# Performance work log

Hardware: AMD Instinct MI355X
Metric: run time of the kernel (lower is better)

The kernel has to match this reference:

```python
import jax, jax.numpy as jnp
import numpy as np

N, E, H, D, L, R = 50000, 800000, 128, 512, 3, 3
BN_EPS = 1e-5


def setup_inputs() -> dict:
    key = jax.random.key(0)
    ks = jax.random.split(key, 10)
    x = jax.random.normal(ks[0], (N, H), jnp.float32)
    edge_src = jax.random.randint(ks[1], (R, E), 0, N, jnp.int32)
    edge_dst = jax.random.randint(ks[2], (R, E), 0, N, jnp.int32)
    conv_W = jax.random.normal(ks[3], (L, R, H, H), jnp.float32) * 0.05
    conv_b = jnp.zeros((L, R, H), jnp.float32)
    fc_W = jax.random.normal(ks[4], (L - 1, H, H), jnp.float32) * 0.05
    fc_b = jnp.zeros((L - 1, H), jnp.float32)
    fc_W_last = jax.random.normal(ks[5], (H, D), jnp.float32) * 0.05
    fc_b_last = jnp.zeros((D,), jnp.float32)
    bn_gamma = jnp.ones((L - 1, H), jnp.float32)
    bn_beta = jnp.zeros((L - 1, H), jnp.float32)
    bn_mean = jax.random.normal(ks[6], (L - 1, H), jnp.float32) * 0.1
    bn_var = jax.random.uniform(ks[7], (L - 1, H), jnp.float32, 0.5, 1.5)
    return {"x": x, "edge_src": edge_src, "edge_dst": edge_dst,
            "conv_W": conv_W, "conv_b": conv_b, "fc_W": fc_W, "fc_b": fc_b,
            "fc_W_last": fc_W_last, "fc_b_last": fc_b_last,
            "bn_gamma": bn_gamma, "bn_beta": bn_beta,
            "bn_mean": bn_mean, "bn_var": bn_var}


def _deg_norm(idx, n, dtype):
    # symmetric GCN norm: 1/sqrt(clamp(deg,1))  (DGL norm='both')
    deg = jax.ops.segment_sum(jnp.ones(idx.shape, dtype), idx, num_segments=n)
    return jax.lax.rsqrt(jnp.maximum(deg, 1.0))


def reference(x, edge_src, edge_dst, conv_W, conv_b, fc_W, fc_b,
              fc_W_last, fc_b_last, bn_gamma, bn_beta, bn_mean, bn_var):
    n = x.shape[0]
    # per-relation degree norms (graph fixed across layers)
    norm_out = [_deg_norm(edge_src[r], n, x.dtype) for r in range(R)]  # src side
    norm_in = [_deg_norm(edge_dst[r], n, x.dtype) for r in range(R)]   # dst side

    for l in range(L):
        # HeteroGraphConv: sum of 3 relation-wise GraphConvs
        h = jnp.zeros((n, conv_W.shape[-1]), x.dtype)
        for r in range(R):
            m = (x * norm_out[r][:, None]) @ conv_W[l, r]          # [N,H] transform first
            agg = jax.ops.segment_sum(m[edge_src[r]], edge_dst[r], num_segments=n)
            h = h + agg * norm_in[r][:, None] + conv_b[l, r]
        if l != L - 1:
            x = h @ fc_W[l] + fc_b[l]
            x = jax.nn.relu(x)
            # BatchNorm1d in eval mode (running stats); dropout = identity in eval
            x = bn_gamma[l] * (x - bn_mean[l]) * jax.lax.rsqrt(bn_var[l] + BN_EPS) + bn_beta[l]
        else:
            x = h @ fc_W_last + fc_b_last
    return x
```

## Files before the change

kernel.cpp:

```cpp
#include <hip/hip_runtime.h>

#define NN 50000
#define EE 800000
#define RR 3
#define HH 128
#define CAP 64
#define NB 128
#define BW 391
#define NBLK 1172
#define SCB 32
#define OVCAP 4096

typedef __attribute__((ext_vector_type(8))) short short8;
typedef __attribute__((ext_vector_type(4))) float f32x4;
typedef unsigned short u16;
typedef unsigned int u32;
typedef unsigned long long u64;

__device__ __forceinline__ float b2f(u16 u){
  unsigned v = ((unsigned)u) << 16;
  return __builtin_bit_cast(float, v);
}
__device__ __forceinline__ u16 f2bu(float f){
  unsigned u = __builtin_bit_cast(unsigned, f);
  u += 0x7fffu + ((u >> 16) & 1u);
  return (u16)(u >> 16);
}

__global__ __launch_bounds__(128) void init_k(u32* __restrict__ xb32, u32* __restrict__ act32){
  int i = threadIdx.x;
  if (i < 64) xb32[(size_t)NN * 64 + i] = 0;
  else act32[(size_t)NN * 64 + (i - 64)] = 0;
}

__global__ __launch_bounds__(256) void bucket_p1(const int* __restrict__ src, const int* __restrict__ dst,
                                                 u32* __restrict__ bktd, u16* __restrict__ bkts,
                                                 int* __restrict__ cnt_d, int* __restrict__ cnt_s,
                                                 u64* __restrict__ ovd, u32* __restrict__ ovs,
                                                 int* __restrict__ ovcur){
  __shared__ int hd[RR * NB];
  __shared__ int hs[RR * NB];
  int tid = threadIdx.x, blk = blockIdx.x;
  for (int k = tid; k < RR * NB; k += 256){ hd[k] = 0; hs[k] = 0; }
  __syncthreads();

  int e0 = (blk * 256 + tid) * 8;
  if (e0 < RR * EE){
    int r = e0 / EE;
#pragma unroll
    for (int h = 0; h < 2; ++h){
      int4 s4 = ((const int4*)src)[(e0 >> 2) + h];
      int4 d4 = ((const int4*)dst)[(e0 >> 2) + h];
      int ss[4] = {s4.x, s4.y, s4.z, s4.w};
      int dd[4] = {d4.x, d4.y, d4.z, d4.w};
#pragma unroll
      for (int j = 0; j < 4; ++j){
        int bd = dd[j] / BW;
        int kd = r * NB + bd;
        u32 sv = (u32)ss[j] | ((u32)(dd[j] - bd * BW) << 16);
        int rk = atomicAdd(&hd[kd], 1);
        if (rk < SCB)
          bktd[((size_t)kd * NBLK + blk) * SCB + rk] = sv;
        else {
          int p = atomicAdd(&ovcur[0], 1);
          if (p < OVCAP) ovd[p] = ((u64)kd << 32) | (u64)sv;
        }
        int bs = ss[j] / BW;
        int ks = r * NB + bs;
        u16 sloc = (u16)(ss[j] - bs * BW);
        int rs = atomicAdd(&hs[ks], 1);
        if (rs < SCB)
          bkts[((size_t)ks * NBLK + blk) * SCB + rs] = sloc;
        else {
          int p = atomicAdd(&ovcur[1], 1);
          if (p < OVCAP) ovs[p] = ((u32)ks << 16) | (u32)sloc;
        }
      }
    }
  }
  __syncthreads();
  for (int k = tid; k < RR * NB; k += 256){
    cnt_d[blk * (RR * NB) + k] = hd[k];
    cnt_s[blk * (RR * NB) + k] = hs[k];
  }
}

__global__ __launch_bounds__(256) void slots_p2(const int* __restrict__ cnt_d, const u32* __restrict__ bktd,
                                                const u64* __restrict__ ovd, const int* __restrict__ ovcur,
                                                u16* __restrict__ slots, int* __restrict__ cnt_in){
  __shared__ int cur[BW];
  int k = blockIdx.x, tid = threadIdx.x;
  int r = k / NB, b = k % NB, d0 = b * BW;
  for (int i = tid; i < BW; i += 256) cur[i] = 0;
  __syncthreads();
  for (int blk = tid; blk < NBLK; blk += 256){
    int c = cnt_d[blk * (RR * NB) + k]; if (c > SCB) c = SCB;
    const u32* buf = bktd + ((size_t)k * NBLK + blk) * SCB;
    for (int t = 0; t < c; ++t){
      u32 pl = buf[t];
      int dl = (int)(pl >> 16), s = (int)(pl & 0xffffu);
      int p = atomicAdd(&cur[dl], 1);
      if (p < CAP) slots[((size_t)r * NN + d0 + dl) * CAP + p] = (u16)s;
    }
  }
  int nov = ovcur[0]; if (nov > OVCAP) nov = OVCAP;
  for (int t = tid; t < nov; t += 256){
    u64 e = ovd[t];
    if ((int)(e >> 32) == k){
      u32 pl = (u32)e;
      int dl = (int)(pl >> 16), s = (int)(pl & 0xffffu);
      int p = atomicAdd(&cur[dl], 1);
      if (p < CAP) slots[((size_t)r * NN + d0 + dl) * CAP + p] = (u16)s;
    }
  }
  __syncthreads();
  for (int i = tid; i < BW; i += 256){
    int d = d0 + i;
    if (d < NN) cnt_in[r * NN + d] = cur[i];
  }
}

__global__ __launch_bounds__(256) void hist_p2(const int* __restrict__ cnt_s, const u16* __restrict__ bkts,
                                               const u32* __restrict__ ovs, const int* __restrict__ ovcur,
                                               float* __restrict__ nout){
  __shared__ int cur[BW];
  int k = blockIdx.x, tid = threadIdx.x;
  int r = k / NB, b = k % NB, d0 = b * BW;
  for (int i = tid; i < BW; i += 256) cur[i] = 0;
  __syncthreads();
  for (int blk = tid; blk < NBLK; blk += 256){
    int c = cnt_s[blk * (RR * NB) + k]; if (c > SCB) c = SCB;
    const u16* buf = bkts + ((size_t)k * NBLK + blk) * SCB;
    for (int t = 0; t < c; ++t)
      atomicAdd(&cur[buf[t]], 1);
  }
  int nov = ovcur[1]; if (nov > OVCAP) nov = OVCAP;
  for (int t = tid; t < nov; t += 256){
    u32 e = ovs[t];
    if ((int)(e >> 16) == k)
      atomicAdd(&cur[e & 0xffffu], 1);
  }
  __syncthreads();
  for (int i = tid; i < BW; i += 256){
    int s = d0 + i;
    if (s < NN){
      int c = cur[i]; if (c < 1) c = 1;
      nout[r * NN + s] = rsqrtf((float)c);
    }
  }
}

__global__ __launch_bounds__(256) void norms2_k(const int* __restrict__ cin,
                                                float* __restrict__ nin, float* __restrict__ nout,
                                                u16* __restrict__ slots){
  int i = blockIdx.x * 256 + threadIdx.x;
  if (i >= RR * NN) return;
  int a = cin[i];
  int c = a; if (c > CAP) c = CAP;
  int n8 = (c + 7) & ~7;
  u16* sl = slots + (size_t)i * CAP;
  for (int p = c; p < n8; ++p) sl[p] = (u16)NN;
  if (a < 1) a = 1;
  nin[i] = rsqrtf((float)a);
  if (i == 0) nout[RR * NN] = 1.0f;
}

__global__ __launch_bounds__(256) void cvt_bf16(const float* __restrict__ in, u16* __restrict__ out, int n4){
  int i = blockIdx.x * 256 + threadIdx.x;
  if (i >= n4) return;
  float4 v = ((const float4*)in)[i];
  ushort4 o; o.x = f2bu(v.x); o.y = f2bu(v.y); o.z = f2bu(v.z); o.w = f2bu(v.w);
  ((ushort4*)out)[i] = o;
}

__global__ __launch_bounds__(256) void pack_bf(const float* __restrict__ B, u16* __restrict__ Bp,
                                               int K, int nc, int total){
  int i = blockIdx.x * 256 + threadIdx.x;
  if (i >= total) return;
  int per = K * nc;
  int b = i / per, rem = i % per;
  int k = rem / nc, n = rem % nc;
  Bp[b * per + ((k >> 3) * nc + n) * 8 + (k & 7)] = f2bu(B[i]);
}

__global__ __launch_bounds__(256) void gather_agg(
    const u16* __restrict__ xin, const u16* __restrict__ slots,
    const int* __restrict__ cin, const float* __restrict__ nin,
    const float* __restrict__ nout, u16* __restrict__ agg)
{
  int tid = threadIdx.x;
  int lane = tid & 63;
  int ql = lane & 15;
  int qb = lane & 48;
  int r = blockIdx.y;
  int row = blockIdx.x * 16 + (tid >> 4);
  int rNN = r * NN;
  const u16* sl = slots + ((size_t)rNN + row) * CAP;
  int cnt = cin[rNN + row]; if (cnt > CAP) cnt = CAP;
  int n8 = (cnt + 7) & ~7;
  float a[8];
#pragma unroll
  for (int k = 0; k < 8; ++k) a[k] = 0.f;

  u32 w = (u32)sl[ql];
  for (int base = 0; base < n8; base += 16){
    u32 wn = 0u;
    if (base + 16 < n8) wn = (u32)sl[base + 16 + ql];
#pragma unroll
    for (int gstep = 0; gstep < 16; gstep += 8){
      if (base + gstep < n8){
        int uu[8]; float cf[8]; short8 vv[8];
#pragma unroll
        for (int j = 0; j < 8; ++j)
          uu[j] = __shfl((int)w, qb + gstep + j);
#pragma unroll
        for (int j = 0; j < 8; ++j)
          vv[j] = *(const short8*)(xin + (size_t)uu[j] * HH + ql * 8);
#pragma unroll
        for (int j = 0; j < 8; ++j)
          cf[j] = nout[rNN + uu[j]];
#pragma unroll
        for (int j = 0; j < 8; ++j){
          float c = cf[j];
#pragma unroll
          for (int k = 0; k < 8; ++k)
            a[k] += c * b2f((u16)vv[j][k]);
        }
      }
    }
    w = wn;
  }
  float sc = nin[rNN + row];
  short8 o;
#pragma unroll
  for (int k = 0; k < 8; ++k) o[k] = (short)f2bu(sc * a[k]);
  *(short8*)(agg + ((size_t)rNN + row) * HH + ql * 8) = o;
}

template<int MODE>
__global__ __launch_bounds__(256) void dense_layer(
    const u16* __restrict__ agg,
    const u16* __restrict__ Wc, const float* __restrict__ bc,
    const u16* __restrict__ Wf, const float* __restrict__ bfc,
    const float* __restrict__ g, const float* __restrict__ be,
    const float* __restrict__ mu, const float* __restrict__ va,
    u16* __restrict__ out_bf, float* __restrict__ out_f)
{
  __shared__ u16 tile[64][136];
  int tid = threadIdx.x, wave = tid >> 6, lane = tid & 63;
  int q = lane >> 4, l15 = lane & 15;
  int nb = blockIdx.x * 64;
  f32x4 zf = {0.f, 0.f, 0.f, 0.f};
  f32x4 acc[8];
#pragma unroll
  for (int ct = 0; ct < 8; ++ct) acc[ct] = zf;

  for (int r = 0; r < RR; ++r){
#pragma unroll
    for (int p = 0; p < 4; ++p){
      int chunk = p * 256 + tid;
      int rw = chunk >> 4, cc = chunk & 15;
      int node = nb + rw;
      if (node >= NN) node = NN - 1;
      short8 v = *(const short8*)(agg + ((size_t)r * NN + node) * HH + cc * 8);
      *(short8*)&tile[rw][cc * 8] = v;
    }
    __syncthreads();
    const short8* bp = (const short8*)(Wc + (size_t)r * HH * HH);
#pragma unroll
    for (int kb = 0; kb < 4; ++kb){
      short8 a = *(const short8*)&tile[wave * 16 + l15][kb * 32 + q * 8];
#pragma unroll
      for (int ct = 0; ct < 8; ++ct){
        short8 b = bp[(kb * 4 + q) * HH + ct * 16 + l15];
        acc[ct] = __builtin_amdgcn_mfma_f32_16x16x32_bf16(a, b, acc[ct], 0, 0, 0);
      }
    }
    __syncthreads();
  }

#pragma unroll
  for (int ct = 0; ct < 8; ++ct){
    int col = ct * 16 + l15;
    float badd = bc[col] + bc[HH + col] + bc[2 * HH + col];
#pragma unroll
    for (int i = 0; i < 4; ++i)
      tile[wave * 16 + q * 4 + i][col] = f2bu(acc[ct][i] + badd);
  }
  __syncthreads();

  if (MODE == 0){
    f32x4 a2[8];
#pragma unroll
    for (int ct = 0; ct < 8; ++ct) a2[ct] = zf;
    const short8* bp = (const short8*)Wf;
#pragma unroll
    for (int kb = 0; kb < 4; ++kb){
      short8 a = *(const short8*)&tile[wave * 16 + l15][kb * 32 + q * 8];
#pragma unroll
      for (int ct = 0; ct < 8; ++ct){
        short8 b = bp[(kb * 4 + q) * HH + ct * 16 + l15];
        a2[ct] = __builtin_amdgcn_mfma_f32_16x16x32_bf16(a, b, a2[ct], 0, 0, 0);
      }
    }
#pragma unroll
    for (int ct = 0; ct < 8; ++ct){
      int col = ct * 16 + l15;
      float bb = bfc[col];
      float s0 = g[col] * rsqrtf(va[col] + 1e-5f);
      float m0 = mu[col], b0 = be[col];
#pragma unroll
      for (int i = 0; i < 4; ++i){
        int node = nb + wave * 16 + q * 4 + i;
        if (node < NN){
          float v = a2[ct][i] + bb;
          v = fmaxf(v, 0.f);
          v = (v - m0) * s0 + b0;
          out_bf[(size_t)node * HH + col] = f2bu(v);
        }
      }
    }
  } else {
    f32x4 a2[4][8];
#pragma unroll
    for (int rt = 0; rt < 4; ++rt)
#pragma unroll
      for (int ct = 0; ct < 8; ++ct) a2[rt][ct] = zf;
    const short8* bp = (const short8*)Wf;
#pragma unroll
    for (int kb = 0; kb < 4; ++kb){
      int cbase = (kb * 4 + q) * 512 + wave * 128;
#pragma unroll
      for (int rt = 0; rt < 4; ++rt){
        short8 a = *(const short8*)&tile[rt * 16 + l15][kb * 32 + q * 8];
#pragma unroll
        for (int ct = 0; ct < 8; ++ct){
          short8 b = bp[cbase + ct * 16 + l15];
          a2[rt][ct] = __builtin_amdgcn_mfma_f32_16x16x32_bf16(a, b, a2[rt][ct], 0, 0, 0);
        }
      }
    }
#pragma unroll
    for (int rt = 0; rt < 4; ++rt)
#pragma unroll
    for (int ct = 0; ct < 8; ++ct){
      int col = wave * 128 + ct * 16 + l15;
      float bb = bfc[col];
#pragma unroll
      for (int i = 0; i < 4; ++i){
        int node = nb + rt * 16 + q * 4 + i;
        if (node < NN) out_f[(size_t)node * 512 + col] = a2[rt][ct][i] + bb;
      }
    }
  }
}

extern "C" void kernel_launch(void* const* d_in, const int* in_sizes, int n_in,
                              void* d_out, int out_size, void* d_ws, size_t ws_size,
                              hipStream_t stream){
  const float* x_in  = (const float*)d_in[0];
  const int* esrc    = (const int*)d_in[1];
  const int* edst    = (const int*)d_in[2];
  const float* convW = (const float*)d_in[3];
  const float* convB = (const float*)d_in[4];
  const float* fcW   = (const float*)d_in[5];
  const float* fcB   = (const float*)d_in[6];
  const float* fcWl  = (const float*)d_in[7];
  const float* fcBl  = (const float*)d_in[8];
  const float* bng   = (const float*)d_in[9];
  const float* bnb   = (const float*)d_in[10];
  const float* bnm   = (const float*)d_in[11];
  const float* bnv   = (const float*)d_in[12];

  char* w = (char*)d_ws;
  size_t off = 0;
  auto alloc = [&](size_t bytes) -> char* {
    char* p = w + off;
    off += (bytes + 255) & ~(size_t)255;
    return p;
  };
  size_t BKTD_B = (size_t)RR * NB * NBLK * SCB * 4;
  size_t BKTS_B = (size_t)RR * NB * NBLK * SCB * 2;
  size_t AGG_B  = (size_t)RR * NN * HH * 2;
  size_t XB_B   = (size_t)(NN + 1) * HH * 2;
  char* regionA = alloc(BKTD_B + BKTS_B);
  u32* bktd = (u32*)regionA;
  u16* bkts = (u16*)(regionA + BKTD_B);
  u16* agg  = (u16*)regionA;
  u16* xb   = (u16*)(regionA + ((AGG_B + 255) & ~(size_t)255));
  u16* act  = (u16*)(regionA + ((AGG_B + XB_B + 511) & ~(size_t)255));

  int* cnt_d   = (int*)alloc((size_t)NBLK * RR * NB * 4);
  int* cnt_s   = (int*)alloc((size_t)NBLK * RR * NB * 4);
  int* cnt_in  = (int*)alloc((size_t)RR * NN * 4);
  float* nin   = (float*)alloc((size_t)RR * NN * 4);
  float* nout  = (float*)alloc((size_t)(RR * NN + 1) * 4);
  u16* slots   = (u16*)alloc((size_t)RR * NN * CAP * 2);
  u64* ovd     = (u64*)alloc((size_t)OVCAP * 8);
  u32* ovs     = (u32*)alloc((size_t)OVCAP * 4);
  int* ovcur   = (int*)alloc(256);
  u16* convWp  = (u16*)alloc((size_t)3 * 384 * 128 * 2);
  u16* fcWp    = (u16*)alloc((size_t)2 * 128 * 128 * 2);
  u16* fcWlp   = (u16*)alloc((size_t)128 * 512 * 2);

  const int TPB = 256;
  hipMemsetAsync(ovcur, 0, 8, stream);
  bucket_p1<<<NBLK, TPB, 0, stream>>>(esrc, edst, bktd, bkts, cnt_d, cnt_s, ovd, ovs, ovcur);
  slots_p2<<<RR * NB, TPB, 0, stream>>>(cnt_d, bktd, ovd, ovcur, slots, cnt_in);
  hist_p2<<<RR * NB, TPB, 0, stream>>>(cnt_s, bkts, ovs, ovcur, nout);
  norms2_k<<<(RR * NN + TPB - 1) / TPB, TPB, 0, stream>>>(cnt_in, nin, nout, slots);
  init_k<<<1, 128, 0, stream>>>((u32*)xb, (u32*)act);
  cvt_bf16<<<(NN * HH / 4 + TPB - 1) / TPB, TPB, 0, stream>>>(x_in, xb, NN * HH / 4);
  pack_bf<<<(3 * 384 * 128 + TPB - 1) / TPB, TPB, 0, stream>>>(convW, convWp, 384, 128, 3 * 384 * 128);
  pack_bf<<<(2 * 128 * 128 + TPB - 1) / TPB, TPB, 0, stream>>>(fcW, fcWp, 128, 128, 2 * 128 * 128);
  pack_bf<<<(128 * 512 + TPB - 1) / TPB, TPB, 0, stream>>>(fcWl, fcWlp, 128, 512, 128 * 512);

  int gx = (NN + 63) / 64;
  dim3 ggrid(NN / 16, RR);

  gather_agg<<<ggrid, TPB, 0, stream>>>(xb, slots, cnt_in, nin, nout, agg);
  dense_layer<0><<<gx, TPB, 0, stream>>>(agg,
      convWp + (size_t)0 * 384 * 128, convB + 0 * 384,
      fcWp + (size_t)0 * 128 * 128, fcB + 0 * 128,
      bng + 0 * 128, bnb + 0 * 128, bnm + 0 * 128, bnv + 0 * 128, act, nullptr);
  gather_agg<<<ggrid, TPB, 0, stream>>>(act, slots, cnt_in, nin, nout, agg);
  dense_layer<0><<<gx, TPB, 0, stream>>>(agg,
      convWp + (size_t)1 * 384 * 128, convB + 1 * 384,
      fcWp + (size_t)1 * 128 * 128, fcB + 1 * 128,
      bng + 1 * 128, bnb + 1 * 128, bnm + 1 * 128, bnv + 1 * 128, act, nullptr);
  gather_agg<<<ggrid, TPB, 0, stream>>>(act, slots, cnt_in, nin, nout, agg);
  dense_layer<1><<<gx, TPB, 0, stream>>>(agg,
      convWp + (size_t)2 * 384 * 128, convB + 2 * 384,
      fcWlp, fcBl,
      nullptr, nullptr, nullptr, nullptr, nullptr, (float*)d_out);
}
```

Before: 601.0 us.

## Fold conv and fc weights into merged matrices, single GEMM per dense layer

Precomputes merged weights Wm = convW[l,r] @ fcW[l] (and @ fcW_last for the final layer) plus merged biases on the device, so each dense layer performs one K=384 GEMM per output tile instead of two chained GEMMs. The dense kernel is retiled to 32-row blocks with 4 waves splitting rows and columns, and the last layer's 512 columns are spread across a second grid dimension. This removes the intermediate bf16 round-trip through shared memory and the second MFMA pass. In exchange, the final layer does more MFMA work because K=384 now maps straight to 512 columns, and rounding differs slightly since the product is taken before bf16 conversion.

```diff
diff --git a/kernel.cpp b/kernel.cpp
--- a/kernel.cpp
+++ b/kernel.cpp
@@ -173,14 +173,55 @@
   ((ushort4*)out)[i] = o;
 }
 
-__global__ __launch_bounds__(256) void pack_bf(const float* __restrict__ B, u16* __restrict__ Bp,
-                                               int K, int nc, int total){
+__global__ __launch_bounds__(256) void mergew(const float* __restrict__ convW, const float* __restrict__ fcW,
+                                              const float* __restrict__ fcWl,
+                                              u16* __restrict__ Wm01, u16* __restrict__ Wm2){
   int i = blockIdx.x * 256 + threadIdx.x;
-  if (i >= total) return;
-  int per = K * nc;
-  int b = i / per, rem = i % per;
-  int k = rem / nc, n = rem % nc;
-  Bp[b * per + ((k >> 3) * nc + n) * 8 + (k & 7)] = f2bu(B[i]);
+  const int N01 = 2 * RR * 128 * 128;
+  if (i < N01){
+    int l = i / (RR * 128 * 128), rem = i % (RR * 128 * 128);
+    int r = rem / (128 * 128), kc = rem % (128 * 128);
+    int k = kc / 128, c = kc % 128;
+    const float* A = convW + (((size_t)l * RR + r) * 128 + k) * 128;
+    const float* B = fcW + (size_t)l * 128 * 128 + c;
+    float s = 0.f;
+#pragma unroll 4
+    for (int t = 0; t < 128; ++t) s += A[t] * B[(size_t)t * 128];
+    Wm01[((size_t)l * RR + r) * 128 * 128 + ((size_t)(k >> 3) * 128 + c) * 8 + (k & 7)] = f2bu(s);
+  } else if (i < N01 + RR * 128 * 512){
+    int j = i - N01;
+    int r = j / (128 * 512), kc = j % (128 * 512);
+    int k = kc / 512, c = kc % 512;
+    const float* A = convW + (((size_t)2 * RR + r) * 128 + k) * 128;
+    const float* B = fcWl + c;
+    float s = 0.f;
+#pragma unroll 4
+    for (int t = 0; t < 128; ++t) s += A[t] * B[(size_t)t * 512];
+    Wm2[(size_t)r * 128 * 512 + ((size_t)(k >> 3) * 512 + c) * 8 + (k & 7)] = f2bu(s);
+  }
+}
+
+__global__ __launch_bounds__(256) void mergeb(const float* __restrict__ convB, const float* __restrict__ fcW,
+                                              const float* __restrict__ fcB, const float* __restrict__ fcWl,
+                                              const float* __restrict__ fcBl, float* __restrict__ bm){
+  int i = blockIdx.x * 256 + threadIdx.x;
+  if (i < 256){
+    int l = i >> 7, c = i & 127;
+    float s = fcB[l * 128 + c];
+    for (int t = 0; t < 128; ++t){
+      float bs = convB[(l * RR + 0) * 128 + t] + convB[(l * RR + 1) * 128 + t] + convB[(l * RR + 2) * 128 + t];
+      s += bs * fcW[(size_t)l * 128 * 128 + (size_t)t * 128 + c];
+    }
+    bm[i] = s;
+  } else if (i < 768){
+    int c = i - 256;
+    float s = fcBl[c];
+    for (int t = 0; t < 128; ++t){
+      float bs = convB[(2 * RR + 0) * 128 + t] + convB[(2 * RR + 1) * 128 + t] + convB[(2 * RR + 2) * 128 + t];
+      s += bs * fcWl[(size_t)t * 512 + c];
+    }
+    bm[i] = s;
+  }
 }
 
 __global__ __launch_bounds__(256) void gather_agg(
@@ -238,26 +279,29 @@
 }
 
 template<int MODE>
-__global__ __launch_bounds__(256) void dense_layer(
-    const u16* __restrict__ agg,
-    const u16* __restrict__ Wc, const float* __restrict__ bc,
-    const u16* __restrict__ Wf, const float* __restrict__ bfc,
+__global__ __launch_bounds__(256) void dense_m(
+    const u16* __restrict__ agg, const u16* __restrict__ Wm, const float* __restrict__ bm,
     const float* __restrict__ g, const float* __restrict__ be,
     const float* __restrict__ mu, const float* __restrict__ va,
     u16* __restrict__ out_bf, float* __restrict__ out_f)
 {
-  __shared__ u16 tile[64][136];
+  const int NC = MODE ? 512 : 128;
+  __shared__ u16 tile[32][136];
   int tid = threadIdx.x, wave = tid >> 6, lane = tid & 63;
   int q = lane >> 4, l15 = lane & 15;
-  int nb = blockIdx.x * 64;
+  int rh = wave & 1, ch = wave >> 1;
+  int nb = blockIdx.x * 32;
+  int cs = blockIdx.y;
+  int cbase = cs * 128 + ch * 64;
   f32x4 zf = {0.f, 0.f, 0.f, 0.f};
-  f32x4 acc[8];
-#pragma unroll
-  for (int ct = 0; ct < 8; ++ct) acc[ct] = zf;
+  f32x4 acc[4];
+#pragma unroll
+  for (int ct = 0; ct < 4; ++ct) acc[ct] = zf;
 
   for (int r = 0; r < RR; ++r){
-#pragma unroll
-    for (int p = 0; p < 4; ++p){
+    if (r) __syncthreads();
+#pragma unroll
+    for (int p = 0; p < 2; ++p){
       int chunk = p * 256 + tid;
       int rw = chunk >> 4, cc = chunk & 15;
       int node = nb + rw;
@@ -266,54 +310,30 @@
       *(short8*)&tile[rw][cc * 8] = v;
     }
     __syncthreads();
-    const short8* bp = (const short8*)(Wc + (size_t)r * HH * HH);
+    const short8* bpr = (const short8*)(Wm + (size_t)r * HH * NC);
 #pragma unroll
     for (int kb = 0; kb < 4; ++kb){
-      short8 a = *(const short8*)&tile[wave * 16 + l15][kb * 32 + q * 8];
-#pragma unroll
-      for (int ct = 0; ct < 8; ++ct){
-        short8 b = bp[(kb * 4 + q) * HH + ct * 16 + l15];
+      short8 a = *(const short8*)&tile[rh * 16 + l15][kb * 32 + q * 8];
+#pragma unroll
+      for (int ct = 0; ct < 4; ++ct){
+        short8 b = bpr[(kb * 4 + q) * NC + cbase + ct * 16 + l15];
         acc[ct] = __builtin_amdgcn_mfma_f32_16x16x32_bf16(a, b, acc[ct], 0, 0, 0);
       }
     }
-    __syncthreads();
-  }
-
-#pragma unroll
-  for (int ct = 0; ct < 8; ++ct){
-    int col = ct * 16 + l15;
-    float badd = bc[col] + bc[HH + col] + bc[2 * HH + col];
-#pragma unroll
-    for (int i = 0; i < 4; ++i)
-      tile[wave * 16 + q * 4 + i][col] = f2bu(acc[ct][i] + badd);
-  }
-  __syncthreads();
+  }
 
   if (MODE == 0){
-    f32x4 a2[8];
-#pragma unroll
-    for (int ct = 0; ct < 8; ++ct) a2[ct] = zf;
-    const short8* bp = (const short8*)Wf;
-#pragma unroll
-    for (int kb = 0; kb < 4; ++kb){
-      short8 a = *(const short8*)&tile[wave * 16 + l15][kb * 32 + q * 8];
-#pragma unroll
-      for (int ct = 0; ct < 8; ++ct){
-        short8 b = bp[(kb * 4 + q) * HH + ct * 16 + l15];
-        a2[ct] = __builtin_amdgcn_mfma_f32_16x16x32_bf16(a, b, a2[ct], 0, 0, 0);
-      }
-    }
-#pragma unroll
-    for (int ct = 0; ct < 8; ++ct){
-      int col = ct * 16 + l15;
-      float bb = bfc[col];
+#pragma unroll
+    for (int ct = 0; ct < 4; ++ct){
+      int col = cbase + ct * 16 + l15;
+      float bb = bm[col];
       float s0 = g[col] * rsqrtf(va[col] + 1e-5f);
       float m0 = mu[col], b0 = be[col];
 #pragma unroll
       for (int i = 0; i < 4; ++i){
-        int node = nb + wave * 16 + q * 4 + i;
+        int node = nb + rh * 16 + q * 4 + i;
         if (node < NN){
-          float v = a2[ct][i] + bb;
+          float v = acc[ct][i] + bb;
           v = fmaxf(v, 0.f);
           v = (v - m0) * s0 + b0;
           out_bf[(size_t)node * HH + col] = f2bu(v);
@@ -321,35 +341,14 @@
       }
     }
   } else {
-    f32x4 a2[4][8];
-#pragma unroll
-    for (int rt = 0; rt < 4; ++rt)
-#pragma unroll
-      for (int ct = 0; ct < 8; ++ct) a2[rt][ct] = zf;
-    const short8* bp = (const short8*)Wf;
-#pragma unroll
-    for (int kb = 0; kb < 4; ++kb){
-      int cbase = (kb * 4 + q) * 512 + wave * 128;
-#pragma unroll
-      for (int rt = 0; rt < 4; ++rt){
-        short8 a = *(const short8*)&tile[rt * 16 + l15][kb * 32 + q * 8];
-#pragma unroll
-        for (int ct = 0; ct < 8; ++ct){
-          short8 b = bp[cbase + ct * 16 + l15];
-          a2[rt][ct] = __builtin_amdgcn_mfma_f32_16x16x32_bf16(a, b, a2[rt][ct], 0, 0, 0);
-        }
-      }
-    }
-#pragma unroll
-    for (int rt = 0; rt < 4; ++rt)
-#pragma unroll
-    for (int ct = 0; ct < 8; ++ct){
-      int col = wave * 128 + ct * 16 + l15;
-      float bb = bfc[col];
+#pragma unroll
+    for (int ct = 0; ct < 4; ++ct){
+      int col = cbase + ct * 16 + l15;
+      float bb = bm[col];
 #pragma unroll
       for (int i = 0; i < 4; ++i){
-        int node = nb + rt * 16 + q * 4 + i;
-        if (node < NN) out_f[(size_t)node * 512 + col] = a2[rt][ct][i] + bb;
+        int node = nb + rh * 16 + q * 4 + i;
+        if (node < NN) out_f[(size_t)node * 512 + col] = acc[ct][i] + bb;
       }
     }
   }
@@ -399,9 +398,9 @@
   u64* ovd     = (u64*)alloc((size_t)OVCAP * 8);
   u32* ovs     = (u32*)alloc((size_t)OVCAP * 4);
   int* ovcur   = (int*)alloc(256);
-  u16* convWp  = (u16*)alloc((size_t)3 * 384 * 128 * 2);
-  u16* fcWp    = (u16*)alloc((size_t)2 * 128 * 128 * 2);
-  u16* fcWlp   = (u16*)alloc((size_t)128 * 512 * 2);
+  u16* Wm01    = (u16*)alloc((size_t)2 * RR * 128 * 128 * 2);
+  u16* Wm2     = (u16*)alloc((size_t)RR * 128 * 512 * 2);
+  float* bm    = (float*)alloc((size_t)768 * 4);
 
   const int TPB = 256;
   hipMemsetAsync(ovcur, 0, 8, stream);
@@ -411,26 +410,23 @@
   norms2_k<<<(RR * NN + TPB - 1) / TPB, TPB, 0, stream>>>(cnt_in, nin, nout, slots);
   init_k<<<1, 128, 0, stream>>>((u32*)xb, (u32*)act);
   cvt_bf16<<<(NN * HH / 4 + TPB - 1) / TPB, TPB, 0, stream>>>(x_in, xb, NN * HH / 4);
-  pack_bf<<<(3 * 384 * 128 + TPB - 1) / TPB, TPB, 0, stream>>>(convW, convWp, 384, 128, 3 * 384 * 128);
-  pack_bf<<<(2 * 128 * 128 + TPB - 1) / TPB, TPB, 0, stream>>>(fcW, fcWp, 128, 128, 2 * 128 * 128);
-  pack_bf<<<(128 * 512 + TPB - 1) / TPB, TPB, 0, stream>>>(fcWl, fcWlp, 128, 512, 128 * 512);
-
-  int gx = (NN + 63) / 64;
+  {
+    int total = 2 * RR * 128 * 128 + RR * 128 * 512;
+    mergew<<<(total + TPB - 1) / TPB, TPB, 0, stream>>>(convW, fcW, fcWl, Wm01, Wm2);
+    mergeb<<<3, TPB, 0, stream>>>(convB, fcW, fcB, fcWl, fcBl, bm);
+  }
+
   dim3 ggrid(NN / 16, RR);
+  dim3 dgrid0((NN + 31) / 32, 1);
+  dim3 dgrid1((NN + 31) / 32, 4);
 
   gather_agg<<<ggrid, TPB, 0, stream>>>(xb, slots, cnt_in, nin, nout, agg);
-  dense_layer<0><<<gx, TPB, 0, stream>>>(agg,
-      convWp + (size_t)0 * 384 * 128, convB + 0 * 384,
-      fcWp + (size_t)0 * 128 * 128, fcB + 0 * 128,
+  dense_m<0><<<dgrid0, TPB, 0, stream>>>(agg, Wm01 + (size_t)0 * RR * 128 * 128, bm + 0,
       bng + 0 * 128, bnb + 0 * 128, bnm + 0 * 128, bnv + 0 * 128, act, nullptr);
   gather_agg<<<ggrid, TPB, 0, stream>>>(act, slots, cnt_in, nin, nout, agg);
-  dense_layer<0><<<gx, TPB, 0, stream>>>(agg,
-      convWp + (size_t)1 * 384 * 128, convB + 1 * 384,
-      fcWp + (size_t)1 * 128 * 128, fcB + 1 * 128,
+  dense_m<0><<<dgrid0, TPB, 0, stream>>>(agg, Wm01 + (size_t)1 * RR * 128 * 128, bm + 128,
       bng + 1 * 128, bnb + 1 * 128, bnm + 1 * 128, bnv + 1 * 128, act, nullptr);
   gather_agg<<<ggrid, TPB, 0, stream>>>(act, slots, cnt_in, nin, nout, agg);
-  dense_layer<1><<<gx, TPB, 0, stream>>>(agg,
-      convWp + (size_t)2 * 384 * 128, convB + 2 * 384,
-      fcWlp, fcBl,
+  dense_m<1><<<dgrid1, TPB, 0, stream>>>(agg, Wm2, bm + 256,
       nullptr, nullptr, nullptr, nullptr, nullptr, (float*)d_out);
 }
```

After: 576.1 us. -4.1%, faster.
